# Kernel tuning notes

Measured on AMD Instinct MI355X. Metric: run time of the kernel, lower is better.

## Reference

```python
import jax, jax.numpy as jnp
import numpy as np

LEVELS = [(128, 128), (64, 64), (32, 32), (16, 16)]  # (h, w) per level
NUM_HEADS = 8
NUM_LEVELS = 4
NUM_POINTS = 4
EMBED_DIMS = 256


def _bilinear_sample(img, gx, gy):
    """grid_sample(mode='bilinear', padding_mode='zeros', align_corners=False).
    img: (B, H, W, C); gx, gy: (B, N) in [-1, 1]. Returns (B, N, C)."""
    B, H, W, C = img.shape
    x = ((gx + 1.0) * W - 1.0) * 0.5
    y = ((gy + 1.0) * H - 1.0) * 0.5
    x0 = jnp.floor(x)
    y0 = jnp.floor(y)
    wx1 = x - x0
    wy1 = y - y0
    flat = img.reshape(B, H * W, C)

    def gather(xf, yf, w):
        xi = xf.astype(jnp.int32)
        yi = yf.astype(jnp.int32)
        valid = (xi >= 0) & (xi < W) & (yi >= 0) & (yi < H)
        idx = jnp.clip(yi, 0, H - 1) * W + jnp.clip(xi, 0, W - 1)
        v = jnp.take_along_axis(flat, idx[..., None], axis=1)
        return v * (w * valid)[..., None]

    return (gather(x0, y0, (1 - wx1) * (1 - wy1))
            + gather(x0 + 1, y0, wx1 * (1 - wy1))
            + gather(x0, y0 + 1, (1 - wx1) * wy1)
            + gather(x0 + 1, y0 + 1, wx1 * wy1))


def _msda(value, sampling_locations, attention_weights):
    """value: (bs, nv, nh, dh); sampling_locations: (bs, nq, nh, L, P, 2);
    attention_weights: (bs, nq, nh, L, P). Returns (bs, nq, nh*dh)."""
    bs, nv, nh, dh = value.shape
    nq = sampling_locations.shape[1]
    P = sampling_locations.shape[4]
    grids = 2.0 * sampling_locations - 1.0
    out = jnp.zeros((bs * nh, nq, dh), value.dtype)
    start = 0
    for l, (h, w) in enumerate(LEVELS):
        v = value[:, start:start + h * w]                      # (bs, h*w, nh, dh)
        start += h * w
        v = v.transpose(0, 2, 1, 3).reshape(bs * nh, h, w, dh)
        g = grids[:, :, :, l].transpose(0, 2, 1, 3, 4).reshape(bs * nh, nq * P, 2)
        s = _bilinear_sample(v, g[..., 0], g[..., 1]).reshape(bs * nh, nq, P, dh)
        wgt = attention_weights[:, :, :, l].transpose(0, 2, 1, 3).reshape(bs * nh, nq, P)
        out = out + jnp.einsum('bqpd,bqp->bqd', s, wgt)
    return out.reshape(bs, nh, nq, dh).transpose(0, 2, 1, 3).reshape(bs, nq, nh * dh)


def setup_inputs() -> dict:
    key = jax.random.key(0)
    ks = jax.random.split(key, 12)
    bs, nq, D = 2, sum(h * w for h, w in LEVELS), EMBED_DIMS
    spatial_shapes = jnp.array(LEVELS, dtype=jnp.int32)
    starts = np.cumsum([0] + [h * w for h, w in LEVELS[:-1]])
    return {
        'query': jax.random.normal(ks[0], (bs, nq, D), jnp.float32),
        'value': jax.random.normal(ks[1], (bs, nq, D), jnp.float32),
        'reference_points': jax.random.uniform(ks[2], (bs, nq, NUM_LEVELS, 2), jnp.float32),
        'spatial_shapes': spatial_shapes,
        'level_start_index': jnp.asarray(starts, dtype=jnp.int32),
        'Wv': jax.random.normal(ks[3], (D, D), jnp.float32) * 0.02,
        'bv': jnp.zeros((D,), jnp.float32),
        'Wo': jax.random.normal(ks[4], (D, NUM_HEADS * NUM_LEVELS * NUM_POINTS * 2), jnp.float32) * 0.02,
        'bo': jax.random.normal(ks[5], (NUM_HEADS * NUM_LEVELS * NUM_POINTS * 2,), jnp.float32) * 0.5,
        'Wa': jax.random.normal(ks[6], (D, NUM_HEADS * NUM_LEVELS * NUM_POINTS), jnp.float32) * 0.02,
        'ba': jnp.zeros((NUM_HEADS * NUM_LEVELS * NUM_POINTS,), jnp.float32),
        'Wout': jax.random.normal(ks[7], (D, D), jnp.float32) * 0.02,
        'bout': jnp.zeros((D,), jnp.float32),
    }


def reference(query, value, reference_points, spatial_shapes, level_start_index,
              Wv, bv, Wo, bo, Wa, ba, Wout, bout):
    bs, nq, D = query.shape
    nv = value.shape[1]
    nh, L, P = NUM_HEADS, NUM_LEVELS, NUM_POINTS
    dh = D // nh
    identity = query

    v = (value @ Wv + bv).reshape(bs, nv, nh, dh)
    offs = (query @ Wo + bo).reshape(bs, nq, nh, L, P, 2)
    attw = jax.nn.softmax((query @ Wa + ba).reshape(bs, nq, nh, L * P), axis=-1)
    attw = attw.reshape(bs, nq, nh, L, P)

    # offset_normalizer = (w, h) per level
    norm = jnp.stack([spatial_shapes[:, 1], spatial_shapes[:, 0]], -1).astype(query.dtype)
    sampling_locations = (reference_points[:, :, None, :, None, :]
                          + offs / norm[None, None, None, :, None, :])

    out = _msda(v, sampling_locations, attw)
    out = out @ Wout + bout
    return out + identity  # dropout is identity in eval
```

## Files before the change

kernel.cpp:

```cpp
#include <hip/hip_runtime.h>
#include <hip/hip_fp16.h>

#define BS 2
#define NQ 21760
#define NV 21760
#define DIM 256
#define NH 8
#define DH 32
#define NL 4
#define NP 4

typedef __attribute__((ext_vector_type(8))) _Float16 f16x8;
typedef __attribute__((ext_vector_type(4))) float f32x4;

__device__ __forceinline__ unsigned short f2h(float f) {
    return __half_as_ushort(__float2half(f));
}
__device__ __forceinline__ float h2f(unsigned short s) {
    return __half2float(__ushort_as_half(s));
}

__global__ __launch_bounds__(64) void k_wprep(
    const float* __restrict__ Wo, const float* __restrict__ Wa,
    const float* __restrict__ Wv, const float* __restrict__ Wout,
    unsigned short* __restrict__ wsw)
{
    const int tile = blockIdx.x;
    const int lane = threadIdx.x;
    const float* W; int N, nb, kb;
    if (tile < 192) { nb = tile >> 3; kb = tile & 7;
        if (nb < 16) { W = Wo; N = 256; } else { W = Wa; N = 128; nb -= 16; } }
    else if (tile < 320) { int tt = tile - 192; nb = tt >> 3; kb = tt & 7; W = Wv;   N = 256; }
    else               { int tt = tile - 320; nb = tt >> 3; kb = tt & 7; W = Wout; N = 256; }
    const int quad = lane >> 4, l15 = lane & 15;
    const int col = nb * 16 + l15;
    unsigned int pk[4];
#pragma unroll
    for (int jj = 0; jj < 4; jj++) {
        int k0 = kb * 32 + quad * 8 + jj * 2;
        pk[jj] = (unsigned int)f2h(W[(size_t)k0 * N + col])
               | ((unsigned int)f2h(W[(size_t)(k0 + 1) * N + col]) << 16);
    }
    *(uint4*)(wsw + (size_t)tile * 512 + lane * 8) = *(const uint4*)pk;
}

__device__ __forceinline__ void stage32_f32(const float* __restrict__ src,
                                            unsigned short* __restrict__ As)
{
    const int t = threadIdx.x;
    const int colg = t & 63;
    const int row0 = t >> 6;
#pragma unroll
    for (int i = 0; i < 8; i++) {
        int row = row0 + i * 4;
        float4 f = ((const float4*)(src + (size_t)row * 256))[colg];
        uint2 p;
        p.x = (unsigned int)f2h(f.x) | ((unsigned int)f2h(f.y) << 16);
        p.y = (unsigned int)f2h(f.z) | ((unsigned int)f2h(f.w) << 16);
        *(uint2*)&As[row * 264 + colg * 4] = p;
    }
}
__device__ __forceinline__ void stage32_h16(const unsigned short* __restrict__ src,
                                            unsigned short* __restrict__ As)
{
    const int t = threadIdx.x;
    const int colg = t & 63;
    const int row0 = t >> 6;
#pragma unroll
    for (int i = 0; i < 8; i++) {
        int row = row0 + i * 4;
        uint2 u = ((const uint2*)(src + (size_t)row * 256))[colg];
        *(uint2*)&As[row * 264 + colg * 4] = u;
    }
}

template<int M>
__device__ __forceinline__ void gemm32(const unsigned short* __restrict__ As,
                                       const unsigned short* __restrict__ wswb,
                                       int mt0, f32x4 acc[][2], int lane)
{
    const int quad = lane >> 4, l15 = lane & 15;
#pragma unroll
    for (int kh = 0; kh < 2; kh++) {
        f16x8 aw[M][4];
#pragma unroll
        for (int m = 0; m < M; m++)
#pragma unroll
            for (int j = 0; j < 4; j++)
                aw[m][j] = *(const f16x8*)(wswb +
                    ((((mt0 + m) * 8 + kh * 4 + j) << 9) + (lane << 3)));
#pragma unroll
        for (int j = 0; j < 4; j++) {
            const int kb = kh * 4 + j;
            f16x8 dq[2];
#pragma unroll
            for (int n = 0; n < 2; n++)
                dq[n] = *(const f16x8*)&As[(n * 16 + l15) * 264 + kb * 32 + quad * 8];
#pragma unroll
            for (int m = 0; m < M; m++)
#pragma unroll
                for (int n = 0; n < 2; n++)
                    acc[m][n] = __builtin_amdgcn_mfma_f32_16x16x32_f16(aw[m][j], dq[n], acc[m][n], 0, 0, 0);
        }
    }
}

__global__ __launch_bounds__(256) void k_proj(
    const float* __restrict__ value,
    const float* __restrict__ query,
    const float* __restrict__ refp,
    const unsigned short* __restrict__ wsw,
    const float* __restrict__ bv,
    const float* __restrict__ bo,
    const float* __restrict__ ba,
    unsigned short* __restrict__ v_hm,
    float* __restrict__ locs_ws,
    unsigned short* __restrict__ attw_b)
{
    __shared__ unsigned short As[32 * 264];
    const int t = threadIdx.x;
    const int w = t >> 6, lane = t & 63;
    const int quad = lane >> 4, l15 = lane & 15;

    if (blockIdx.x < 1360) {
        const int tile = blockIdx.x;
        const int r0i = tile * 32;
        const int bb = (tile >= 680);
        const int pix0 = r0i - bb * NV;
        stage32_f32(value + (size_t)r0i * 256, As);
        __syncthreads();
        f32x4 acc[4][2];
#pragma unroll
        for (int m = 0; m < 4; m++)
#pragma unroll
            for (int n = 0; n < 2; n++) acc[m][n] = (f32x4){0.f, 0.f, 0.f, 0.f};
        gemm32<4>(As, wsw + 98304, w * 4, acc, lane);
#pragma unroll
        for (int m = 0; m < 4; m++) {
            const int col = w * 64 + m * 16 + quad * 4;
            const int h = col >> 5, ch = col & 31;
            const float4 bias = *(const float4*)(bv + col);
            unsigned short* __restrict__ vh =
                v_hm + ((size_t)(bb * NH + h) * NV + pix0) * DH + ch;
#pragma unroll
            for (int n = 0; n < 2; n++) {
                f32x4 a = acc[m][n];
                uint2 o;
                o.x = (unsigned int)f2h(a[0] + bias.x)
                    | ((unsigned int)f2h(a[1] + bias.y) << 16);
                o.y = (unsigned int)f2h(a[2] + bias.z)
                    | ((unsigned int)f2h(a[3] + bias.w) << 16);
                *(uint2*)(vh + (size_t)(n * 16 + l15) * DH) = o;
            }
        }
    } else {
        const int qb = blockIdx.x - 1360;
        const int rt = qb >> 1, ch2 = qb & 1;
        const size_t r0 = (size_t)rt * 32;
        stage32_f32(query + r0 * 256, As);
        __syncthreads();
        f32x4 acc[3][2];
#pragma unroll
        for (int m = 0; m < 3; m++)
#pragma unroll
            for (int n = 0; n < 2; n++) acc[m][n] = (f32x4){0.f, 0.f, 0.f, 0.f};
        const int mt0 = ch2 * 12 + w * 3;
        gemm32<3>(As, wsw, mt0, acc, lane);
#pragma unroll
        for (int m = 0; m < 3; m++) {
            const int mt = mt0 + m;
            if (mt < 16) {
                const int c0 = mt * 16 + quad * 4;
                const int l = (c0 >> 3) & 3;
                const float rnorm = 1.f / (float)(128 >> l);
                const float4 bias = *(const float4*)(bo + c0);
#pragma unroll
                for (int n = 0; n < 2; n++) {
                    size_t row = r0 + n * 16 + l15;
                    float2 ref = *(const float2*)(refp + row * 8 + l * 2);
                    f32x4 a = acc[m][n];
                    float4 o;
                    o.x = ref.x + (a[0] + bias.x) * rnorm;
                    o.y = ref.y + (a[1] + bias.y) * rnorm;
                    o.z = ref.x + (a[2] + bias.z) * rnorm;
                    o.w = ref.y + (a[3] + bias.w) * rnorm;
                    *(float4*)(locs_ws + row * 256 + c0) = o;
                }
            } else {
                const int c0 = (mt - 16) * 16 + quad * 4;
                const float4 bias = *(const float4*)(ba + c0);
#pragma unroll
                for (int n = 0; n < 2; n++) {
                    size_t row = r0 + n * 16 + l15;
                    f32x4 a = acc[m][n];
                    float v0 = a[0] + bias.x, v1 = a[1] + bias.y;
                    float v2 = a[2] + bias.z, v3 = a[3] + bias.w;
                    float mm = fmaxf(fmaxf(v0, v1), fmaxf(v2, v3));
                    mm = fmaxf(mm, __shfl_xor(mm, 16, 64));
                    mm = fmaxf(mm, __shfl_xor(mm, 32, 64));
                    float e0 = __expf(v0 - mm), e1 = __expf(v1 - mm);
                    float e2 = __expf(v2 - mm), e3 = __expf(v3 - mm);
                    float s = (e0 + e1) + (e2 + e3);
                    s += __shfl_xor(s, 16, 64);
                    s += __shfl_xor(s, 32, 64);
                    float rs = 1.f / s;
                    uint2 o;
                    o.x = (unsigned int)f2h(e0 * rs) | ((unsigned int)f2h(e1 * rs) << 16);
                    o.y = (unsigned int)f2h(e2 * rs) | ((unsigned int)f2h(e3 * rs) << 16);
                    *(uint2*)(attw_b + row * 128 + c0) = o;
                }
            }
        }
    }
}

__device__ __forceinline__ void acc8(float wf, uint4 d, float* ac)
{
    __half2 p0 = *(__half2*)&d.x;
    __half2 p1 = *(__half2*)&d.y;
    __half2 p2 = *(__half2*)&d.z;
    __half2 p3 = *(__half2*)&d.w;
    ac[0] = fmaf(wf, __half2float(__low2half(p0)),  ac[0]);
    ac[1] = fmaf(wf, __half2float(__high2half(p0)), ac[1]);
    ac[2] = fmaf(wf, __half2float(__low2half(p1)),  ac[2]);
    ac[3] = fmaf(wf, __half2float(__high2half(p1)), ac[3]);
    ac[4] = fmaf(wf, __half2float(__low2half(p2)),  ac[4]);
    ac[5] = fmaf(wf, __half2float(__high2half(p2)), ac[5]);
    ac[6] = fmaf(wf, __half2float(__low2half(p3)),  ac[6]);
    ac[7] = fmaf(wf, __half2float(__high2half(p3)), ac[7]);
}

__global__ __launch_bounds__(256) void k_sample(
    const unsigned short* __restrict__ v_hm,
    const float* __restrict__ locs_ws,
    const unsigned short* __restrict__ attw_b,
    unsigned short* __restrict__ msda_ws)
{
    __shared__ uint4 tap[16 * 2 * 33];
    const int t = threadIdx.x;
    const int bid = blockIdx.x;

    const int xcd  = bid & 7;
    const int slot = bid >> 3;
    const int sub  = (slot >= 680) ? 1 : 0;
    const int chunk = slot - sub * 680;
    const int pair = xcd * 2 + sub;
    const int b = pair & 1;
    const int h = pair >> 1;
    const int q0 = chunk * 32;

#pragma unroll
    for (int i = 0; i < 2; i++) {
        const int item = t + i * 256;
        const int tp = item & 15;
        const int q  = item >> 4;
        const size_t row = (size_t)(b * NQ + q0 + q);
        float2 xy = *(const float2*)(locs_ws + row * 256 + h * 32 + tp * 2);
        float a   = h2f(attw_b[row * 128 + h * 16 + tp]);

        const int l = tp >> 2;
        const int Wl = 128 >> l;
        const float Wf = (float)Wl;
        const int start = (l == 0) ? 0 : (l == 1) ? 16384 : (l == 2) ? 20480 : 21504;
        float x = xy.x * Wf - 0.5f;
        float y = xy.y * Wf - 0.5f;
        float xf = floorf(x), yf = floorf(y);
        int x0 = (int)xf, y0 = (int)yf;
        float wx1 = x - xf, wx0 = 1.f - wx1;
        float wy1 = y - yf, wy0 = 1.f - wy1;
        const int base = min(max(x0, 0), Wl - 2);
        const int sh = x0 - base;
        const float wxA = (sh == 0) ? wx0 : (sh == -1) ? wx1 : 0.f;
        const float wxB = (sh == 0) ? wx1 : (sh == 1)  ? wx0 : 0.f;
#pragma unroll
        for (int dy = 0; dy < 2; dy++) {
            int yi = y0 + dy;
            bool yv = (yi >= 0) && (yi < Wl);
            int yc = min(max(yi, 0), Wl - 1);
            float wY = yv ? a * (dy ? wy1 : wy0) : 0.f;
            uint4 rec;
            rec.x = __float_as_uint(wY * wxA);
            rec.y = __float_as_uint(wY * wxB);
            rec.z = (unsigned int)(start + yc * Wl + base) * 64u;
            rec.w = 0u;
            tap[(tp * 2 + dy) * 33 + q] = rec;
        }
    }
    __syncthreads();

    const int w4   = t >> 6;
    const int lane = t & 63;
    const int ql   = lane >> 3;
    const int g    = lane & 7;
    const int q    = w4 * 8 + ql;
    const bool selA = (g < 4);
    const unsigned int goff = (unsigned int)g * 16u;
    const char* __restrict__ vb =
        (const char*)(v_hm + (size_t)(b * NH + h) * NV * DH);

    float ac[8] = {0.f, 0.f, 0.f, 0.f, 0.f, 0.f, 0.f, 0.f};
#pragma unroll
    for (int it = 0; it < 32; it++) {
        uint4 rec = tap[it * 33 + q];
        float wf = __uint_as_float(selA ? rec.x : rec.y);
        uint4 d = *(const uint4*)(vb + (rec.z + goff));
        acc8(wf, d, ac);
    }
#pragma unroll
    for (int k = 0; k < 8; k++) ac[k] += __shfl_xor(ac[k], 4, 64);
    if (selA) {
        uint4 o;
        o.x = (unsigned int)f2h(ac[0]) | ((unsigned int)f2h(ac[1]) << 16);
        o.y = (unsigned int)f2h(ac[2]) | ((unsigned int)f2h(ac[3]) << 16);
        o.z = (unsigned int)f2h(ac[4]) | ((unsigned int)f2h(ac[5]) << 16);
        o.w = (unsigned int)f2h(ac[6]) | ((unsigned int)f2h(ac[7]) << 16);
        *(uint4*)(msda_ws + (size_t)(b * NQ + q0 + q) * DIM + h * DH + g * 8) = o;
    }
}

__global__ __launch_bounds__(256) void k_out_mfma(
    const unsigned short* __restrict__ msda_ws,
    const unsigned short* __restrict__ wswo,
    const float* __restrict__ bout,
    const float* __restrict__ query,
    float* __restrict__ out)
{
    __shared__ unsigned short As[32 * 264];
    const int t = threadIdx.x;
    const int w = t >> 6, lane = t & 63;
    const int quad = lane >> 4, l15 = lane & 15;
    const size_t r0 = (size_t)blockIdx.x * 32;

    stage32_h16(msda_ws + r0 * 256, As);
    __syncthreads();

    f32x4 acc[4][2];
#pragma unroll
    for (int m = 0; m < 4; m++)
#pragma unroll
        for (int n = 0; n < 2; n++) acc[m][n] = (f32x4){0.f, 0.f, 0.f, 0.f};
    gemm32<4>(As, wswo, w * 4, acc, lane);

#pragma unroll
    for (int m = 0; m < 4; m++) {
        const int c0 = w * 64 + m * 16 + quad * 4;
        const float4 bias = *(const float4*)(bout + c0);
#pragma unroll
        for (int n = 0; n < 2; n++) {
            size_t row = r0 + n * 16 + l15;
            float4 q4 = *(const float4*)(query + row * 256 + c0);
            f32x4 a = acc[m][n];
            float4 o;
            o.x = a[0] + bias.x + q4.x;
            o.y = a[1] + bias.y + q4.y;
            o.z = a[2] + bias.z + q4.z;
            o.w = a[3] + bias.w + q4.w;
            *(float4*)(out + row * 256 + c0) = o;
        }
    }
}

extern "C" void kernel_launch(void* const* d_in, const int* in_sizes, int n_in,
                              void* d_out, int out_size, void* d_ws, size_t ws_size,
                              hipStream_t stream)
{
    const float* query = (const float*)d_in[0];
    const float* value = (const float*)d_in[1];
    const float* refp  = (const float*)d_in[2];
    const float* Wv   = (const float*)d_in[5];
    const float* bv   = (const float*)d_in[6];
    const float* Wo   = (const float*)d_in[7];
    const float* bo   = (const float*)d_in[8];
    const float* Wa   = (const float*)d_in[9];
    const float* ba   = (const float*)d_in[10];
    const float* Wout = (const float*)d_in[11];
    const float* bout = (const float*)d_in[12];
    float* out = (float*)d_out;

    char* ws = (char*)d_ws;
    unsigned short* v_hm = (unsigned short*)ws;    ws += (size_t)BS * NH * NV * DH * 2;
    float* locs_ws = (float*)ws;                   ws += (size_t)BS * NQ * DIM * 4;
    unsigned short* attw_b = (unsigned short*)ws;  ws += (size_t)BS * NQ * 128 * 2;
    unsigned short* msda_ws = (unsigned short*)ws; ws += (size_t)BS * NQ * DIM * 2;
    unsigned short* wsw = (unsigned short*)ws;

    k_wprep   <<<448, 64,  0, stream>>>(Wo, Wa, Wv, Wout, wsw);
    k_proj    <<<4080, 256, 0, stream>>>(value, query, refp, wsw, bv, bo, ba,
                                         v_hm, locs_ws, attw_b);
    k_sample  <<<10880, 256, 0, stream>>>(v_hm, locs_ws, attw_b, msda_ws);
    k_out_mfma<<<1360, 256, 0, stream>>>(msda_ws, wsw + 163840, bout, query, out);
}
```

Baseline: 266.0 us.

## Load GEMM activations directly from global memory, drop LDS staging

The projection and output GEMMs now read their activation fragments straight from global memory into MFMA operand registers, converting to fp16 on the fly, instead of first staging a 32-row tile in shared memory behind a barrier. The query-projection blocks now run both column halves in a loop within one block, which cuts the k_proj grid from 4080 to 2720 blocks and avoids staging the query tile twice. This removes LDS traffic and barriers but makes each wave issue redundant global loads of the same rows, so it relies on L1/L2 caching. It also lowers block-level parallelism in the query path.

```diff
diff --git a/kernel.cpp b/kernel.cpp
--- a/kernel.cpp
+++ b/kernel.cpp
@@ -44,40 +44,10 @@
     *(uint4*)(wsw + (size_t)tile * 512 + lane * 8) = *(const uint4*)pk;
 }
 
-__device__ __forceinline__ void stage32_f32(const float* __restrict__ src,
-                                            unsigned short* __restrict__ As)
-{
-    const int t = threadIdx.x;
-    const int colg = t & 63;
-    const int row0 = t >> 6;
-#pragma unroll
-    for (int i = 0; i < 8; i++) {
-        int row = row0 + i * 4;
-        float4 f = ((const float4*)(src + (size_t)row * 256))[colg];
-        uint2 p;
-        p.x = (unsigned int)f2h(f.x) | ((unsigned int)f2h(f.y) << 16);
-        p.y = (unsigned int)f2h(f.z) | ((unsigned int)f2h(f.w) << 16);
-        *(uint2*)&As[row * 264 + colg * 4] = p;
-    }
-}
-__device__ __forceinline__ void stage32_h16(const unsigned short* __restrict__ src,
-                                            unsigned short* __restrict__ As)
-{
-    const int t = threadIdx.x;
-    const int colg = t & 63;
-    const int row0 = t >> 6;
-#pragma unroll
-    for (int i = 0; i < 8; i++) {
-        int row = row0 + i * 4;
-        uint2 u = ((const uint2*)(src + (size_t)row * 256))[colg];
-        *(uint2*)&As[row * 264 + colg * 4] = u;
-    }
-}
-
 template<int M>
-__device__ __forceinline__ void gemm32(const unsigned short* __restrict__ As,
-                                       const unsigned short* __restrict__ wswb,
-                                       int mt0, f32x4 acc[][2], int lane)
+__device__ __forceinline__ void gemm32_dir_f32(const float* __restrict__ src,
+                                               const unsigned short* __restrict__ wswb,
+                                               int mt0, f32x4 acc[][2], int lane)
 {
     const int quad = lane >> 4, l15 = lane & 15;
 #pragma unroll
@@ -94,8 +64,47 @@
             const int kb = kh * 4 + j;
             f16x8 dq[2];
 #pragma unroll
+            for (int n = 0; n < 2; n++) {
+                const float* p = src + (size_t)(n * 16 + l15) * 256 + kb * 32 + quad * 8;
+                float4 fa = *(const float4*)p;
+                float4 fb = *(const float4*)(p + 4);
+                f16x8 d;
+                d[0] = (_Float16)fa.x; d[1] = (_Float16)fa.y;
+                d[2] = (_Float16)fa.z; d[3] = (_Float16)fa.w;
+                d[4] = (_Float16)fb.x; d[5] = (_Float16)fb.y;
+                d[6] = (_Float16)fb.z; d[7] = (_Float16)fb.w;
+                dq[n] = d;
+            }
+#pragma unroll
+            for (int m = 0; m < M; m++)
+#pragma unroll
+                for (int n = 0; n < 2; n++)
+                    acc[m][n] = __builtin_amdgcn_mfma_f32_16x16x32_f16(aw[m][j], dq[n], acc[m][n], 0, 0, 0);
+        }
+    }
+}
+template<int M>
+__device__ __forceinline__ void gemm32_dir_h16(const unsigned short* __restrict__ src,
+                                               const unsigned short* __restrict__ wswb,
+                                               int mt0, f32x4 acc[][2], int lane)
+{
+    const int quad = lane >> 4, l15 = lane & 15;
+#pragma unroll
+    for (int kh = 0; kh < 2; kh++) {
+        f16x8 aw[M][4];
+#pragma unroll
+        for (int m = 0; m < M; m++)
+#pragma unroll
+            for (int j = 0; j < 4; j++)
+                aw[m][j] = *(const f16x8*)(wswb +
+                    ((((mt0 + m) * 8 + kh * 4 + j) << 9) + (lane << 3)));
+#pragma unroll
+        for (int j = 0; j < 4; j++) {
+            const int kb = kh * 4 + j;
+            f16x8 dq[2];
+#pragma unroll
             for (int n = 0; n < 2; n++)
-                dq[n] = *(const f16x8*)&As[(n * 16 + l15) * 264 + kb * 32 + quad * 8];
+                dq[n] = *(const f16x8*)(src + (size_t)(n * 16 + l15) * 256 + kb * 32 + quad * 8);
 #pragma unroll
             for (int m = 0; m < M; m++)
 #pragma unroll
@@ -117,24 +126,21 @@
     float* __restrict__ locs_ws,
     unsigned short* __restrict__ attw_b)
 {
-    __shared__ unsigned short As[32 * 264];
     const int t = threadIdx.x;
     const int w = t >> 6, lane = t & 63;
     const int quad = lane >> 4, l15 = lane & 15;
 
     if (blockIdx.x < 1360) {
         const int tile = blockIdx.x;
-        const int r0i = tile * 32;
         const int bb = (tile >= 680);
-        const int pix0 = r0i - bb * NV;
-        stage32_f32(value + (size_t)r0i * 256, As);
-        __syncthreads();
+        const int pix0 = tile * 32 - bb * NV;
+        const float* src = value + (size_t)tile * 32 * 256;
         f32x4 acc[4][2];
 #pragma unroll
         for (int m = 0; m < 4; m++)
 #pragma unroll
             for (int n = 0; n < 2; n++) acc[m][n] = (f32x4){0.f, 0.f, 0.f, 0.f};
-        gemm32<4>(As, wsw + 98304, w * 4, acc, lane);
+        gemm32_dir_f32<4>(src, wsw + 98304, w * 4, acc, lane);
 #pragma unroll
         for (int m = 0; m < 4; m++) {
             const int col = w * 64 + m * 16 + quad * 4;
@@ -154,60 +160,61 @@
             }
         }
     } else {
-        const int qb = blockIdx.x - 1360;
-        const int rt = qb >> 1, ch2 = qb & 1;
+        const int rt = blockIdx.x - 1360;
         const size_t r0 = (size_t)rt * 32;
-        stage32_f32(query + r0 * 256, As);
-        __syncthreads();
-        f32x4 acc[3][2];
-#pragma unroll
-        for (int m = 0; m < 3; m++)
-#pragma unroll
-            for (int n = 0; n < 2; n++) acc[m][n] = (f32x4){0.f, 0.f, 0.f, 0.f};
-        const int mt0 = ch2 * 12 + w * 3;
-        gemm32<3>(As, wsw, mt0, acc, lane);
-#pragma unroll
-        for (int m = 0; m < 3; m++) {
-            const int mt = mt0 + m;
-            if (mt < 16) {
-                const int c0 = mt * 16 + quad * 4;
-                const int l = (c0 >> 3) & 3;
-                const float rnorm = 1.f / (float)(128 >> l);
-                const float4 bias = *(const float4*)(bo + c0);
-#pragma unroll
-                for (int n = 0; n < 2; n++) {
-                    size_t row = r0 + n * 16 + l15;
-                    float2 ref = *(const float2*)(refp + row * 8 + l * 2);
-                    f32x4 a = acc[m][n];
-                    float4 o;
-                    o.x = ref.x + (a[0] + bias.x) * rnorm;
-                    o.y = ref.y + (a[1] + bias.y) * rnorm;
-                    o.z = ref.x + (a[2] + bias.z) * rnorm;
-                    o.w = ref.y + (a[3] + bias.w) * rnorm;
-                    *(float4*)(locs_ws + row * 256 + c0) = o;
-                }
-            } else {
-                const int c0 = (mt - 16) * 16 + quad * 4;
-                const float4 bias = *(const float4*)(ba + c0);
-#pragma unroll
-                for (int n = 0; n < 2; n++) {
-                    size_t row = r0 + n * 16 + l15;
-                    f32x4 a = acc[m][n];
-                    float v0 = a[0] + bias.x, v1 = a[1] + bias.y;
-                    float v2 = a[2] + bias.z, v3 = a[3] + bias.w;
-                    float mm = fmaxf(fmaxf(v0, v1), fmaxf(v2, v3));
-                    mm = fmaxf(mm, __shfl_xor(mm, 16, 64));
-                    mm = fmaxf(mm, __shfl_xor(mm, 32, 64));
-                    float e0 = __expf(v0 - mm), e1 = __expf(v1 - mm);
-                    float e2 = __expf(v2 - mm), e3 = __expf(v3 - mm);
-                    float s = (e0 + e1) + (e2 + e3);
-                    s += __shfl_xor(s, 16, 64);
-                    s += __shfl_xor(s, 32, 64);
-                    float rs = 1.f / s;
-                    uint2 o;
-                    o.x = (unsigned int)f2h(e0 * rs) | ((unsigned int)f2h(e1 * rs) << 16);
-                    o.y = (unsigned int)f2h(e2 * rs) | ((unsigned int)f2h(e3 * rs) << 16);
-                    *(uint2*)(attw_b + row * 128 + c0) = o;
+        const float* src = query + r0 * 256;
+#pragma unroll
+        for (int pass = 0; pass < 2; pass++) {
+            const int mt0 = pass * 12 + w * 3;
+            f32x4 acc[3][2];
+#pragma unroll
+            for (int m = 0; m < 3; m++)
+#pragma unroll
+                for (int n = 0; n < 2; n++) acc[m][n] = (f32x4){0.f, 0.f, 0.f, 0.f};
+            gemm32_dir_f32<3>(src, wsw, mt0, acc, lane);
+#pragma unroll
+            for (int m = 0; m < 3; m++) {
+                const int mt = mt0 + m;
+                if (mt < 16) {
+                    const int c0 = mt * 16 + quad * 4;
+                    const int l = (c0 >> 3) & 3;
+                    const float rnorm = 1.f / (float)(128 >> l);
+                    const float4 bias = *(const float4*)(bo + c0);
+#pragma unroll
+                    for (int n = 0; n < 2; n++) {
+                        size_t row = r0 + n * 16 + l15;
+                        float2 ref = *(const float2*)(refp + row * 8 + l * 2);
+                        f32x4 a = acc[m][n];
+                        float4 o;
+                        o.x = ref.x + (a[0] + bias.x) * rnorm;
+                        o.y = ref.y + (a[1] + bias.y) * rnorm;
+                        o.z = ref.x + (a[2] + bias.z) * rnorm;
+                        o.w = ref.y + (a[3] + bias.w) * rnorm;
+                        *(float4*)(locs_ws + row * 256 + c0) = o;
+                    }
+                } else {
+                    const int c0 = (mt - 16) * 16 + quad * 4;
+                    const float4 bias = *(const float4*)(ba + c0);
+#pragma unroll
+                    for (int n = 0; n < 2; n++) {
+                        size_t row = r0 + n * 16 + l15;
+                        f32x4 a = acc[m][n];
+                        float v0 = a[0] + bias.x, v1 = a[1] + bias.y;
+                        float v2 = a[2] + bias.z, v3 = a[3] + bias.w;
+                        float mm = fmaxf(fmaxf(v0, v1), fmaxf(v2, v3));
+                        mm = fmaxf(mm, __shfl_xor(mm, 16, 64));
+                        mm = fmaxf(mm, __shfl_xor(mm, 32, 64));
+                        float e0 = __expf(v0 - mm), e1 = __expf(v1 - mm);
+                        float e2 = __expf(v2 - mm), e3 = __expf(v3 - mm);
+                        float s = (e0 + e1) + (e2 + e3);
+                        s += __shfl_xor(s, 16, 64);
+                        s += __shfl_xor(s, 32, 64);
+                        float rs = 1.f / s;
+                        uint2 o;
+                        o.x = (unsigned int)f2h(e0 * rs) | ((unsigned int)f2h(e1 * rs) << 16);
+                        o.y = (unsigned int)f2h(e2 * rs) | ((unsigned int)f2h(e3 * rs) << 16);
+                        *(uint2*)(attw_b + row * 128 + c0) = o;
+                    }
                 }
             }
         }
@@ -325,21 +332,17 @@
     const float* __restrict__ query,
     float* __restrict__ out)
 {
-    __shared__ unsigned short As[32 * 264];
     const int t = threadIdx.x;
     const int w = t >> 6, lane = t & 63;
     const int quad = lane >> 4, l15 = lane & 15;
     const size_t r0 = (size_t)blockIdx.x * 32;
 
-    stage32_h16(msda_ws + r0 * 256, As);
-    __syncthreads();
-
     f32x4 acc[4][2];
 #pragma unroll
     for (int m = 0; m < 4; m++)
 #pragma unroll
         for (int n = 0; n < 2; n++) acc[m][n] = (f32x4){0.f, 0.f, 0.f, 0.f};
-    gemm32<4>(As, wswo, w * 4, acc, lane);
+    gemm32_dir_h16<4>(msda_ws + r0 * 256, wswo, w * 4, acc, lane);
 
 #pragma unroll
     for (int m = 0; m < 4; m++) {
@@ -385,7 +388,7 @@
     unsigned short* wsw = (unsigned short*)ws;
 
     k_wprep   <<<448, 64,  0, stream>>>(Wo, Wa, Wv, Wout, wsw);
-    k_proj    <<<4080, 256, 0, stream>>>(value, query, refp, wsw, bv, bo, ba,
+    k_proj    <<<2720, 256, 0, stream>>>(value, query, refp, wsw, bv, bo, ba,
                                          v_hm, locs_ws, attw_b);
     k_sample  <<<10880, 256, 0, stream>>>(v_hm, locs_ws, attw_b, msda_ws);
     k_out_mfma<<<1360, 256, 0, stream>>>(msda_ws, wsw + 163840, bout, query, out);
```

New measurement: 300.2 us. 1.13x slower.
